# Performance work log

Measured on AMD Instinct MI355X. Metric: run time of the kernel, lower is better.

Reference implementation:

```python
import jax, jax.numpy as jnp
import numpy as np

BETA = 0.25
GAMMA = 0.9
EPS = 1e-05
B, H, W, D, K = 64, 32, 32, 256, 1024


def setup_inputs() -> dict:
    key = jax.random.key(0)
    k1, k2 = jax.random.split(key)
    return {
        "inputs": jax.random.normal(k1, (B, H, W, D), dtype=jnp.float32),
        "codebook": jax.random.normal(k2, (D, K), dtype=jnp.float32),
        "ema_hidden_cluster": jnp.zeros((K,), dtype=jnp.float32),
        "ema_hidden_dw": jnp.zeros((D, K), dtype=jnp.float32),
        "counter": 1,  # counter after increment (fresh state: 0 + 1)
    }


def reference(inputs, codebook, ema_hidden_cluster, ema_hidden_dw, counter):
    d, k = codebook.shape
    flat = inputs.reshape(-1, d)  # [N, D]
    distances = (
        jnp.sum(jnp.square(flat), 1, keepdims=True)
        - 2.0 * jnp.matmul(flat, codebook)
        + jnp.sum(jnp.square(codebook), 0, keepdims=True)
    )
    encoding_indices = jnp.argmin(distances, axis=1)  # [N]
    encodings = jax.nn.one_hot(encoding_indices, k, dtype=distances.dtype)  # [N, K]
    flat_quantized = jnp.take(codebook, encoding_indices, axis=1).swapaxes(1, 0)  # [N, D]
    quantized = flat_quantized.reshape(inputs.shape)
    loss = BETA * jnp.mean(jnp.square(jax.lax.stop_gradient(quantized) - inputs))

    # --- EMA codebook update (training=True path) ---
    decay = jnp.float32(GAMMA)
    one = jnp.float32(1.0)
    bias = one - jnp.power(decay, counter)
    cluster_size = jnp.sum(encodings, axis=0)  # [K]
    hid_cs = ema_hidden_cluster * decay + cluster_size * (one - decay)
    avg_cs = hid_cs / bias
    dw = jnp.matmul(flat.T, encodings)  # [D, K]
    hid_dw = ema_hidden_dw * decay + dw * (one - decay)
    avg_dw = hid_dw / bias
    n = jnp.sum(avg_cs)
    smoothed_cs = (avg_cs + EPS) / (n + k * EPS) * n
    new_codebook = avg_dw / smoothed_cs[None, :]

    ste = inputs + jax.lax.stop_gradient(quantized - inputs)
    avg_probs = jnp.mean(encodings, 0)
    perplexity = jnp.exp(-jnp.sum(avg_probs * jnp.log(avg_probs + 1e-10)))
    return (ste, perplexity, loss, new_codebook)
```

## Files before the change

kernel.cpp:

```cpp
#include <hip/hip_runtime.h>

#define N 65536
#define D 256
#define K 1024
#define BETA 0.25f
#define GAMMA 0.9f
#define EPS 1e-5f

#define QBLOCKS 512
#define DWROWS 64

#define OFF_INDICES 0
#define OFF_PERM    262144
#define OFF_COUNTS  524288
#define OFF_CNORM   528384
#define OFF_OFFSETS 532480
#define OFF_CURSOR  536576
#define OFF_SMOOTH  540672
#define OFF_LOSSP   544768
#define OFF_CBT     546816
#define OFF_CBE     1595392

typedef __bf16 bf16x8 __attribute__((ext_vector_type(8)));
typedef short  s16x8  __attribute__((ext_vector_type(8)));
typedef float  f32x4  __attribute__((ext_vector_type(4)));

__device__ inline unsigned short f32_to_bf16_rn(float f) {
    unsigned int u = __float_as_uint(f);
    unsigned int r = u + 0x7fffu + ((u >> 16) & 1u);
    return (unsigned short)(r >> 16);
}

__device__ inline f32x4 mfma16(s16x8 a, s16x8 b, f32x4 c) {
    return __builtin_amdgcn_mfma_f32_16x16x32_bf16(
        __builtin_bit_cast(bf16x8, a), __builtin_bit_cast(bf16x8, b), c, 0, 0, 0);
}

__device__ __forceinline__ void stage16(const s16x8* __restrict__ g, s16x8* l) {
    __builtin_amdgcn_global_load_lds(
        (const __attribute__((address_space(1))) void*)g,
        (__attribute__((address_space(3))) void*)l, 16, 0, 0);
}

__global__ __launch_bounds__(256) void pack_cb(const float* __restrict__ cb,
                                               float* __restrict__ cbT,
                                               s16x8* __restrict__ cbEp,
                                               float* __restrict__ cnorm) {
    const int ct = blockIdx.x >> 2;
    const int c2 = blockIdx.x & 3;
#pragma unroll
    for (int it = 0; it < 2; ++it) {
        int u = it * 256 + threadIdx.x;
        int frgc = u >> 7;
        int ks = (u >> 6) & 1;
        int L = u & 63;
        int c = ct * 64 + frgc * 16 + (L & 15);
        int d0 = c2 * 64 + (ks * 4 + (L >> 4)) * 8;
        float v[8];
        s16x8 hv, lv;
        float ss = 0.f;
#pragma unroll
        for (int j = 0; j < 8; ++j) {
            float f = cb[(size_t)(d0 + j) * K + c];
            v[j] = f;
            unsigned short h = f32_to_bf16_rn(f);
            hv[j] = (short)h;
            lv[j] = (short)f32_to_bf16_rn(f - __uint_as_float((unsigned)h << 16));
            ss = fmaf(f, f, ss);
        }
        *(float4*)&cbT[(size_t)c * D + d0]     = make_float4(v[0], v[1], v[2], v[3]);
        *(float4*)&cbT[(size_t)c * D + d0 + 4] = make_float4(v[4], v[5], v[6], v[7]);
        cbEp[(size_t)(ct * 8 + c2) * 512 + u]     = hv;
        cbEp[(size_t)(ct * 8 + 4 + c2) * 512 + u] = lv;
        atomicAdd(&cnorm[c], ss);
    }
}

__global__ __launch_bounds__(256, 1) void argmin_mfma_kernel(
        const float* __restrict__ x,
        const s16x8* __restrict__ cbEp,
        const float* __restrict__ cnorm,
        int* __restrict__ indices) {
    __shared__ s16x8 Bs[2][2048];

    const int tid = threadIdx.x;
    const int lane = tid & 63;
    const int w = tid >> 6;
    const int r0 = blockIdx.x * 128;
    const int row16 = lane & 15;
    const int quad = lane >> 4;

#pragma unroll
    for (int i = 0; i < 8; ++i)
        stage16(cbEp + i * 256 + tid, &Bs[0][i * 256 + w * 64]);

    s16x8 Ah[2][8], Al[2][8];
#pragma unroll
    for (int frg = 0; frg < 2; ++frg) {
#pragma unroll
        for (int kb8 = 0; kb8 < 8; ++kb8) {
            const float* src = &x[(size_t)(r0 + w * 32 + frg * 16 + row16) * D
                                  + kb8 * 32 + quad * 8];
            float4 v0 = *(const float4*)src;
            float4 v1 = *(const float4*)(src + 4);
            float f[8] = {v0.x, v0.y, v0.z, v0.w, v1.x, v1.y, v1.z, v1.w};
            s16x8 hv, lv;
#pragma unroll
            for (int j = 0; j < 8; ++j) {
                unsigned short h = f32_to_bf16_rn(f[j]);
                hv[j] = (short)h;
                lv[j] = (short)f32_to_bf16_rn(f[j] - __uint_as_float((unsigned)h << 16));
            }
            Ah[frg][kb8] = hv;
            Al[frg][kb8] = lv;
        }
    }

    float minv[2][4];
    int   mini[2][4];
#pragma unroll
    for (int frg = 0; frg < 2; ++frg)
#pragma unroll
        for (int reg = 0; reg < 4; ++reg) { minv[frg][reg] = 3.4e38f; mini[frg][reg] = 0; }

    for (int ct = 0; ct < 16; ++ct) {
        f32x4 acc[2][4];
#pragma unroll
        for (int frg = 0; frg < 2; ++frg)
#pragma unroll
            for (int fc = 0; fc < 4; ++fc) acc[frg][fc] = (f32x4){0.f, 0.f, 0.f, 0.f};

#pragma unroll
        for (int g = 0; g < 2; ++g) {
            __syncthreads();
            const bool has_next = !(ct == 15 && g == 1);
            if (has_next) {
                const int nct = (g == 1) ? ct + 1 : ct;
                const int ng  = (g == 1) ? 0 : 1;
                const size_t gb = (size_t)(nct * 8 + ng * 4) * 512;
#pragma unroll
                for (int i = 0; i < 8; ++i)
                    stage16(cbEp + gb + i * 256 + tid, &Bs[g ^ 1][i * 256 + w * 64]);
            }
#pragma unroll
            for (int h = 0; h < 4; ++h) {
#pragma unroll
                for (int ks = 0; ks < 2; ++ks) {
                    const int ksb = h * 2 + ks;
#pragma unroll
                    for (int fc = 0; fc < 4; ++fc) {
                        s16x8 b = Bs[g][h * 512 + (fc * 2 + ks) * 64 + lane];
#pragma unroll
                        for (int frg = 0; frg < 2; ++frg) {
                            acc[frg][fc] = mfma16(Ah[frg][ksb], b, acc[frg][fc]);
                            if (g == 0)
                                acc[frg][fc] = mfma16(Al[frg][ksb], b, acc[frg][fc]);
                        }
                    }
                }
            }
        }
#pragma unroll
        for (int fc = 0; fc < 4; ++fc) {
            int col = ct * 64 + fc * 16 + row16;
            float cn = cnorm[col];
#pragma unroll
            for (int frg = 0; frg < 2; ++frg)
#pragma unroll
                for (int reg = 0; reg < 4; ++reg) {
                    float val = fmaf(-2.f, acc[frg][fc][reg], cn);
                    if (val < minv[frg][reg]) { minv[frg][reg] = val; mini[frg][reg] = col; }
                }
        }
    }

#pragma unroll
    for (int mask = 1; mask <= 8; mask <<= 1) {
#pragma unroll
        for (int frg = 0; frg < 2; ++frg)
#pragma unroll
            for (int reg = 0; reg < 4; ++reg) {
                float ov = __shfl_xor(minv[frg][reg], mask, 64);
                int   oi = __shfl_xor(mini[frg][reg], mask, 64);
                if (ov < minv[frg][reg] ||
                    (ov == minv[frg][reg] && oi < mini[frg][reg])) {
                    minv[frg][reg] = ov; mini[frg][reg] = oi;
                }
            }
    }
    if (row16 == 0) {
#pragma unroll
        for (int frg = 0; frg < 2; ++frg)
#pragma unroll
            for (int reg = 0; reg < 4; ++reg)
                indices[r0 + w * 32 + frg * 16 + quad * 4 + reg] = mini[frg][reg];
    }
}

__global__ __launch_bounds__(256) void quantize_kernel(const float* __restrict__ x,
                                                       const float* __restrict__ cbT,
                                                       const int* __restrict__ indices,
                                                       float* __restrict__ ste,
                                                       int* __restrict__ counts,
                                                       float* __restrict__ loss_partial,
                                                       float* __restrict__ dwT) {
    const int gid = blockIdx.x * 256 + threadIdx.x;
    if (gid < (K * D / 4))
        *(float4*)&dwT[(size_t)gid * 4] = make_float4(0.f, 0.f, 0.f, 0.f);

    const int lane = threadIdx.x & 63;
    const int wid = gid >> 6;
    const int nwaves = QBLOCKS * 4;

    float s = 0.f;
    for (int row = wid; row < N; row += nwaves) {
        const int k = indices[row];
        float4 q  = *(const float4*)&cbT[(size_t)k * D + lane * 4];
        float4 xi = *(const float4*)&x[(size_t)row * D + lane * 4];
        *(float4*)&ste[(size_t)row * D + lane * 4] = q;
        float dx = q.x - xi.x, dy = q.y - xi.y, dz = q.z - xi.z, dw = q.w - xi.w;
        s = fmaf(dx, dx, s); s = fmaf(dy, dy, s);
        s = fmaf(dz, dz, s); s = fmaf(dw, dw, s);
        if (lane == 0) atomicAdd(&counts[k], 1);
    }
#pragma unroll
    for (int off = 32; off >= 1; off >>= 1) s += __shfl_down(s, off, 64);
    __shared__ float red[4];
    if (lane == 0) red[threadIdx.x >> 6] = s;
    __syncthreads();
    if (threadIdx.x == 0)
        loss_partial[blockIdx.x] = red[0] + red[1] + red[2] + red[3];
}

__global__ __launch_bounds__(1024) void finalize_kernel(const int* __restrict__ counts,
                                                        const float* __restrict__ ema_c,
                                                        const int* __restrict__ counter,
                                                        const float* __restrict__ loss_partial,
                                                        float* __restrict__ out_perp,
                                                        float* __restrict__ out_loss,
                                                        int* __restrict__ offsets,
                                                        int* __restrict__ cursor,
                                                        float* __restrict__ smoothed) {
    const int k = threadIdx.x;
    __shared__ float fred[1024];
    __shared__ int scan[1024];
    __shared__ float nsum_s;
    __shared__ float ent_s;

    const int c = counts[k];
    const float bias = 1.0f - powf(GAMMA, (float)counter[0]);
    const float hid = fmaf(ema_c[k], GAMMA, (float)c * (1.0f - GAMMA));
    const float avg = hid / bias;

    fred[k] = avg;
    __syncthreads();
    for (int s = 512; s >= 1; s >>= 1) {
        if (k < s) fred[k] += fred[k + s];
        __syncthreads();
    }
    if (k == 0) nsum_s = fred[0];
    __syncthreads();
    const float nsum = nsum_s;

    float p = (float)c * (1.0f / (float)N);
    fred[k] = p * logf(p + 1e-10f);
    __syncthreads();
    for (int s = 512; s >= 1; s >>= 1) {
        if (k < s) fred[k] += fred[k + s];
        __syncthreads();
    }
    if (k == 0) ent_s = fred[0];
    __syncthreads();

    fred[k] = (k < QBLOCKS) ? loss_partial[k] : 0.f;
    __syncthreads();
    for (int s = 512; s >= 1; s >>= 1) {
        if (k < s) fred[k] += fred[k + s];
        __syncthreads();
    }

    scan[k] = c;
    __syncthreads();
    for (int s = 1; s < 1024; s <<= 1) {
        int v = (k >= s) ? scan[k - s] : 0;
        __syncthreads();
        scan[k] += v;
        __syncthreads();
    }
    const int excl = scan[k] - c;
    offsets[k] = excl;
    cursor[k] = excl;

    smoothed[k] = (avg + EPS) / (nsum + (float)K * EPS) * nsum;

    if (k == 0) {
        out_perp[0] = expf(-ent_s);
        out_loss[0] = BETA * fred[0] * (1.0f / ((float)N * (float)D));
    }
}

__global__ __launch_bounds__(256) void scatter_kernel(const int* __restrict__ indices,
                                                      int* __restrict__ cursor,
                                                      int* __restrict__ perm,
                                                      int* __restrict__ skey) {
    const int n = blockIdx.x * 256 + threadIdx.x;
    const int k = indices[n];
    const int pos = atomicAdd(&cursor[k], 1);
    perm[pos] = n;
    skey[pos] = k;
}

__global__ __launch_bounds__(256) void dw_accum_kernel(const float* __restrict__ x,
                                                       const int* __restrict__ perm,
                                                       const int* __restrict__ skey,
                                                       float* __restrict__ dwT) {
    __shared__ int s_rows[DWROWS];
    __shared__ int s_keys[DWROWS + 1];
    const int d = threadIdx.x;
    const int base = blockIdx.x * DWROWS;
    if (threadIdx.x < DWROWS) {
        s_rows[threadIdx.x] = perm[base + threadIdx.x];
        s_keys[threadIdx.x] = skey[base + threadIdx.x];
    }
    if (threadIdx.x == 0) s_keys[DWROWS] = -1;
    __syncthreads();
    float acc = 0.f;
#pragma unroll 4
    for (int i = 0; i < DWROWS; ++i) {
        acc += x[(size_t)s_rows[i] * D + d];
        if (s_keys[i + 1] != s_keys[i]) {
            atomicAdd(&dwT[(size_t)s_keys[i] * D + d], acc);
            acc = 0.f;
        }
    }
}

__global__ __launch_bounds__(256) void codebook_final_kernel(const float* __restrict__ dwT,
                                                             const float* __restrict__ ema_dw,
                                                             const float* __restrict__ smoothed,
                                                             const int* __restrict__ counter,
                                                             float* __restrict__ out_cb) {
    __shared__ float tile[64][65];
    const int d0 = (blockIdx.x & 3) * 64;
    const int k0 = (blockIdx.x >> 2) * 64;
    const int tid = threadIdx.x;
#pragma unroll
    for (int it = 0; it < 16; ++it) {
        int idx = it * 256 + tid;
        int kk = idx >> 6, dd = idx & 63;
        tile[kk][dd] = dwT[(size_t)(k0 + kk) * D + d0 + dd];
    }
    __syncthreads();
    const float bias = 1.0f - powf(GAMMA, (float)counter[0]);
#pragma unroll
    for (int it = 0; it < 16; ++it) {
        int idx = it * 256 + tid;
        int dd = idx >> 6, kk = idx & 63;
        float dwv = tile[kk][dd];
        float hid = fmaf(ema_dw[(size_t)(d0 + dd) * K + k0 + kk], GAMMA,
                         dwv * (1.0f - GAMMA));
        out_cb[(size_t)(d0 + dd) * K + k0 + kk] = (hid / bias) / smoothed[k0 + kk];
    }
}

extern "C" void kernel_launch(void* const* d_in, const int* in_sizes, int n_in,
                              void* d_out, int out_size, void* d_ws, size_t ws_size,
                              hipStream_t stream) {
    const float* x       = (const float*)d_in[0];
    const float* cb      = (const float*)d_in[1];
    const float* ema_c   = (const float*)d_in[2];
    const float* ema_dw  = (const float*)d_in[3];
    const int*   counter = (const int*)d_in[4];

    float* out = (float*)d_out;
    float* ste = out;
    float* out_perp = out + (size_t)N * D;
    float* out_loss = out_perp + 1;
    float* out_cb = out_perp + 2;

    char* ws = (char*)d_ws;
    int* indices  = (int*)(ws + OFF_INDICES);
    int* perm     = (int*)(ws + OFF_PERM);
    int* counts   = (int*)(ws + OFF_COUNTS);
    float* cnorm  = (float*)(ws + OFF_CNORM);
    int* offsets  = (int*)(ws + OFF_OFFSETS);
    int* cursor   = (int*)(ws + OFF_CURSOR);
    float* smooth = (float*)(ws + OFF_SMOOTH);
    float* lossp  = (float*)(ws + OFF_LOSSP);
    float* cbT    = (float*)(ws + OFF_CBT);
    s16x8* cbEp   = (s16x8*)(ws + OFF_CBE);
    int* skey     = (int*)(ws + OFF_CBT);
    float* dwT    = (float*)(ws + OFF_CBE);

    hipMemsetAsync(counts, 0, 2 * K * sizeof(int), stream);

    pack_cb<<<64, 256, 0, stream>>>(cb, cbT, cbEp, cnorm);
    argmin_mfma_kernel<<<N / 128, 256, 0, stream>>>(x, cbEp, cnorm, indices);
    quantize_kernel<<<QBLOCKS, 256, 0, stream>>>(x, cbT, indices, ste, counts, lossp, dwT);
    finalize_kernel<<<1, 1024, 0, stream>>>(counts, ema_c, counter, lossp,
                                            out_perp, out_loss, offsets, cursor, smooth);
    scatter_kernel<<<N / 256, 256, 0, stream>>>(indices, cursor, perm, skey);
    dw_accum_kernel<<<N / DWROWS, 256, 0, stream>>>(x, perm, skey, dwT);
    codebook_final_kernel<<<64, 256, 0, stream>>>(dwT, ema_dw, smooth, counter, out_cb);
}
```

Measured before the change: 344.2 us.

## Split argmin MFMA reduction dimension across wave pairs with LDS partial-sum exchange

The argmin kernel now runs 512 threads per block, with each pair of waves splitting the 256-wide reduction dimension in half. Each wave holds half the A fragments in registers, and the partial dot products are combined through a swizzled LDS exchange buffer before the argmin update. The aim is more waves per CU and lower register pressure, to hide MFMA and load latency. The cost is an extra __syncthreads and an LDS round trip per column tile, plus one wave of each pair sitting idle during the argmin epilogue.

Result: slower. 355.8 us (+3.4%).

```diff
diff --git a/kernel.cpp b/kernel.cpp
--- a/kernel.cpp
+++ b/kernel.cpp
@@ -76,43 +76,45 @@
     }
 }
 
-__global__ __launch_bounds__(256, 1) void argmin_mfma_kernel(
+__global__ __launch_bounds__(512, 2) void argmin_mfma_kernel(
         const float* __restrict__ x,
         const s16x8* __restrict__ cbEp,
         const float* __restrict__ cnorm,
         int* __restrict__ indices) {
-    __shared__ s16x8 Bs[2][2048];
+    __shared__ s16x8 Bs[2][1024];
+    __shared__ float xch[8192];
 
     const int tid = threadIdx.x;
     const int lane = tid & 63;
     const int w = tid >> 6;
+    const int rg = w >> 1;
+    const int kh = w & 1;
     const int r0 = blockIdx.x * 128;
     const int row16 = lane & 15;
     const int quad = lane >> 4;
 
-#pragma unroll
-    for (int i = 0; i < 8; ++i)
-        stage16(cbEp + i * 256 + tid, &Bs[0][i * 256 + w * 64]);
-
-    s16x8 Ah[2][8], Al[2][8];
+    stage16(cbEp + tid, &Bs[0][w << 6]);
+    stage16(cbEp + 2 * 512 + tid, &Bs[0][512 + (w << 6)]);
+
+    s16x8 Ah[2][4], Al[2][4];
 #pragma unroll
     for (int frg = 0; frg < 2; ++frg) {
 #pragma unroll
-        for (int kb8 = 0; kb8 < 8; ++kb8) {
-            const float* src = &x[(size_t)(r0 + w * 32 + frg * 16 + row16) * D
-                                  + kb8 * 32 + quad * 8];
+        for (int j = 0; j < 4; ++j) {
+            const float* src = &x[(size_t)(r0 + rg * 32 + frg * 16 + row16) * D
+                                  + (kh * 4 + j) * 32 + quad * 8];
             float4 v0 = *(const float4*)src;
             float4 v1 = *(const float4*)(src + 4);
             float f[8] = {v0.x, v0.y, v0.z, v0.w, v1.x, v1.y, v1.z, v1.w};
             s16x8 hv, lv;
 #pragma unroll
-            for (int j = 0; j < 8; ++j) {
-                unsigned short h = f32_to_bf16_rn(f[j]);
-                hv[j] = (short)h;
-                lv[j] = (short)f32_to_bf16_rn(f[j] - __uint_as_float((unsigned)h << 16));
+            for (int jj = 0; jj < 8; ++jj) {
+                unsigned short h = f32_to_bf16_rn(f[jj]);
+                hv[jj] = (short)h;
+                lv[jj] = (short)f32_to_bf16_rn(f[jj] - __uint_as_float((unsigned)h << 16));
             }
-            Ah[frg][kb8] = hv;
-            Al[frg][kb8] = lv;
+            Ah[frg][j] = hv;
+            Al[frg][j] = lv;
         }
     }
 
@@ -131,69 +133,90 @@
             for (int fc = 0; fc < 4; ++fc) acc[frg][fc] = (f32x4){0.f, 0.f, 0.f, 0.f};
 
 #pragma unroll
-        for (int g = 0; g < 2; ++g) {
+        for (int p = 0; p < 4; ++p) {
+            const int buf = (ct * 4 + p) & 1;
             __syncthreads();
-            const bool has_next = !(ct == 15 && g == 1);
+            const bool has_next = !(ct == 15 && p == 3);
             if (has_next) {
-                const int nct = (g == 1) ? ct + 1 : ct;
-                const int ng  = (g == 1) ? 0 : 1;
-                const size_t gb = (size_t)(nct * 8 + ng * 4) * 512;
-#pragma unroll
-                for (int i = 0; i < 8; ++i)
-                    stage16(cbEp + gb + i * 256 + tid, &Bs[g ^ 1][i * 256 + w * 64]);
+                const int np  = (p + 1) & 3;
+                const int nct = (p == 3) ? ct + 1 : ct;
+                const int cb0 = ((np >= 2) ? 4 : 0) + (np & 1);
+                const size_t gb = (size_t)(nct * 8 + cb0) * 512;
+                stage16(cbEp + gb + tid, &Bs[buf ^ 1][w << 6]);
+                stage16(cbEp + gb + 2 * 512 + tid, &Bs[buf ^ 1][512 + (w << 6)]);
             }
 #pragma unroll
-            for (int h = 0; h < 4; ++h) {
-#pragma unroll
-                for (int ks = 0; ks < 2; ++ks) {
-                    const int ksb = h * 2 + ks;
-#pragma unroll
-                    for (int fc = 0; fc < 4; ++fc) {
-                        s16x8 b = Bs[g][h * 512 + (fc * 2 + ks) * 64 + lane];
-#pragma unroll
-                        for (int frg = 0; frg < 2; ++frg) {
-                            acc[frg][fc] = mfma16(Ah[frg][ksb], b, acc[frg][fc]);
-                            if (g == 0)
-                                acc[frg][fc] = mfma16(Al[frg][ksb], b, acc[frg][fc]);
-                        }
+            for (int ks = 0; ks < 2; ++ks) {
+                const int ksb = (p & 1) * 2 + ks;
+#pragma unroll
+                for (int fc = 0; fc < 4; ++fc) {
+                    s16x8 b = Bs[buf][kh * 512 + (fc * 2 + ks) * 64 + lane];
+#pragma unroll
+                    for (int frg = 0; frg < 2; ++frg) {
+                        acc[frg][fc] = mfma16(Ah[frg][ksb], b, acc[frg][fc]);
+                        if (p < 2)
+                            acc[frg][fc] = mfma16(Al[frg][ksb], b, acc[frg][fc]);
                     }
                 }
             }
         }
-#pragma unroll
-        for (int fc = 0; fc < 4; ++fc) {
-            int col = ct * 64 + fc * 16 + row16;
-            float cn = cnorm[col];
+
+        if (kh) {
 #pragma unroll
             for (int frg = 0; frg < 2; ++frg)
 #pragma unroll
-                for (int reg = 0; reg < 4; ++reg) {
-                    float val = fmaf(-2.f, acc[frg][fc][reg], cn);
-                    if (val < minv[frg][reg]) { minv[frg][reg] = val; mini[frg][reg] = col; }
+                for (int fc = 0; fc < 4; ++fc) {
+                    const int col = fc * 16 + row16;
+                    const int rowb = frg * 16 + quad * 4;
+                    const int idx = rg * 2048 + col * 32 + (rowb ^ ((col & 7) << 2));
+                    *(f32x4*)&xch[idx] = acc[frg][fc];
                 }
         }
-    }
-
-#pragma unroll
-    for (int mask = 1; mask <= 8; mask <<= 1) {
-#pragma unroll
-        for (int frg = 0; frg < 2; ++frg)
-#pragma unroll
-            for (int reg = 0; reg < 4; ++reg) {
-                float ov = __shfl_xor(minv[frg][reg], mask, 64);
-                int   oi = __shfl_xor(mini[frg][reg], mask, 64);
-                if (ov < minv[frg][reg] ||
-                    (ov == minv[frg][reg] && oi < mini[frg][reg])) {
-                    minv[frg][reg] = ov; mini[frg][reg] = oi;
+        __syncthreads();
+        if (!kh) {
+#pragma unroll
+            for (int fc = 0; fc < 4; ++fc) {
+                const int col16 = fc * 16 + row16;
+                const int col = ct * 64 + col16;
+                const float cn = cnorm[col];
+#pragma unroll
+                for (int frg = 0; frg < 2; ++frg) {
+                    const int rowb = frg * 16 + quad * 4;
+                    const int idx = rg * 2048 + col16 * 32 + (rowb ^ ((col16 & 7) << 2));
+                    f32x4 other = *(const f32x4*)&xch[idx];
+#pragma unroll
+                    for (int reg = 0; reg < 4; ++reg) {
+                        float dot = acc[frg][fc][reg] + other[reg];
+                        float val = fmaf(-2.f, dot, cn);
+                        if (val < minv[frg][reg]) { minv[frg][reg] = val; mini[frg][reg] = col; }
+                    }
                 }
             }
-    }
-    if (row16 == 0) {
-#pragma unroll
-        for (int frg = 0; frg < 2; ++frg)
-#pragma unroll
-            for (int reg = 0; reg < 4; ++reg)
-                indices[r0 + w * 32 + frg * 16 + quad * 4 + reg] = mini[frg][reg];
+        }
+    }
+
+    if (!kh) {
+#pragma unroll
+        for (int mask = 1; mask <= 8; mask <<= 1) {
+#pragma unroll
+            for (int frg = 0; frg < 2; ++frg)
+#pragma unroll
+                for (int reg = 0; reg < 4; ++reg) {
+                    float ov = __shfl_xor(minv[frg][reg], mask, 64);
+                    int   oi = __shfl_xor(mini[frg][reg], mask, 64);
+                    if (ov < minv[frg][reg] ||
+                        (ov == minv[frg][reg] && oi < mini[frg][reg])) {
+                        minv[frg][reg] = ov; mini[frg][reg] = oi;
+                    }
+                }
+        }
+        if (row16 == 0) {
+#pragma unroll
+            for (int frg = 0; frg < 2; ++frg)
+#pragma unroll
+                for (int reg = 0; reg < 4; ++reg)
+                    indices[r0 + rg * 32 + frg * 16 + quad * 4 + reg] = mini[frg][reg];
+        }
     }
 }
 
@@ -395,7 +418,7 @@
     hipMemsetAsync(counts, 0, 2 * K * sizeof(int), stream);
 
     pack_cb<<<64, 256, 0, stream>>>(cb, cbT, cbEp, cnorm);
-    argmin_mfma_kernel<<<N / 128, 256, 0, stream>>>(x, cbEp, cnorm, indices);
+    argmin_mfma_kernel<<<N / 128, 512, 0, stream>>>(x, cbEp, cnorm, indices);
     quantize_kernel<<<QBLOCKS, 256, 0, stream>>>(x, cbT, indices, ste, counts, lossp, dwT);
     finalize_kernel<<<1, 1024, 0, stream>>>(counts, ema_c, counter, lossp,
                                             out_perp, out_loss, offsets, cursor, smooth);
```
